# Optimization experiments

Measured on AMD Instinct MI355X. Metric: run time of the kernel, lower is better.

## Reference

```python
import jax, jax.numpy as jnp
import numpy as np

BASE_THETA = 0.5
K_DOP = 0.2
K_NOR = 0.15
K_SERO = 0.1
DIM = 1024


def setup_inputs() -> dict:
    key = jax.random.key(0)
    ks = jax.random.split(key, 9)
    scale = 1.0 / np.sqrt(DIM)
    x = jax.random.normal(ks[0], (2, 2048, DIM), dtype=jnp.float32)
    Wq = jax.random.normal(ks[1], (DIM, DIM), dtype=jnp.float32) * scale
    bq = jnp.zeros((DIM,), dtype=jnp.float32)
    Wk = jax.random.normal(ks[2], (DIM, DIM), dtype=jnp.float32) * scale
    bk = jnp.zeros((DIM,), dtype=jnp.float32)
    Wv = jax.random.normal(ks[3], (DIM, DIM), dtype=jnp.float32) * scale
    bv = jnp.zeros((DIM,), dtype=jnp.float32)
    Wo = jax.random.normal(ks[4], (DIM, DIM), dtype=jnp.float32) * scale
    bo = jnp.zeros((DIM,), dtype=jnp.float32)
    return {"x": x, "Wq": Wq, "bq": bq, "Wk": Wk, "bk": bk,
            "Wv": Wv, "bv": bv, "Wo": Wo, "bo": bo}


def reference(x, Wq, bq, Wk, bk, Wv, bv, Wo, bo):
    # Projections: torch nn.Linear computes x @ W.T + b
    q = jnp.einsum('bsd,ed->bse', x, Wq) + bq
    k = jnp.einsum('bsd,ed->bse', x, Wk) + bk
    v = jnp.einsum('bsd,ed->bse', x, Wv) + bv
    # Full [B, S, S] scores (no 1/sqrt(d) scaling in the original)
    qk = jnp.einsum('bsd,btd->bst', q, k)
    theta = (BASE_THETA
             + K_DOP * jax.nn.sigmoid(qk)
             + K_NOR * jnp.tanh(qk)
             + K_SERO * jax.nn.relu(qk))
    attn = jax.nn.softmax(theta, axis=-1)
    out = jnp.einsum('bst,btd->bsd', attn, v)
    return jnp.einsum('bsd,ed->bse', out, Wo) + bo
```

## Files before the change

kernel.cpp:

```cpp
#include <hip/hip_runtime.h>
#include <hip/hip_fp16.h>
#include <stdint.h>

typedef _Float16 f16;
typedef __attribute__((ext_vector_type(8))) _Float16 f16x8;
typedef __attribute__((ext_vector_type(4))) _Float16 f16x4;
typedef __attribute__((ext_vector_type(4))) float f32x4;

#define SEQ 2048
#define DIM 1024
#define NBATCH 2
#define MTOT 4096

__global__ void fill_kernel(float* p, float v, int n){
  int i = blockIdx.x * 256 + threadIdx.x;
  if (i < n) p[i] = v;
}

__global__ void cvt_all(const float* __restrict__ x, const float* __restrict__ Wq,
                        const float* __restrict__ Wk, const float* __restrict__ Wv,
                        const float* __restrict__ Wo, const float* __restrict__ bo,
                        f16* __restrict__ x16, f16* __restrict__ Wcat, f16* __restrict__ Wo16,
                        float* __restrict__ rowacc, float* __restrict__ out){
  int b = blockIdx.x;
  if (b >= 8193){
    const long i = (long)(b - 8193) * 256 + threadIdx.x;
    ((float4*)out)[i] = ((const float4*)bo)[i & 255];
    return;
  }
  if (b == 8192){
    float4 z = {0.f, 0.f, 0.f, 0.f};
#pragma unroll
    for (int i = 0; i < 4; i++) ((float4*)rowacc)[threadIdx.x + i * 256] = z;
    return;
  }
  const float* src; f16* dst; int i;
  if (b < 4096){
    src = x; dst = x16; i = b * 256 + threadIdx.x;
  } else {
    int t = (b - 4096) >> 10;
    i = ((b - 4096) & 1023) * 256 + threadIdx.x;
    src = t == 0 ? Wq : t == 1 ? Wk : t == 2 ? Wv : Wo;
    dst = (t == 3) ? Wo16 : Wcat + (size_t)t * DIM * DIM;
  }
  float4 v = ((const float4*)src)[i];
  ((f16x4*)dst)[i] = (f16x4){(f16)v.x, (f16)v.y, (f16)v.z, (f16)v.w};
}

#define GLOAD16(SRC, DST) __builtin_amdgcn_global_load_lds( \
    (__attribute__((address_space(1))) void*)(SRC), \
    (__attribute__((address_space(3))) void*)(DST), 16, 0, 0)

__device__ __forceinline__ float theta_exp(float v){
  const float e1 = __expf(-v);
  const float sg = 1.f / (1.f + e1);
  const float e2 = e1 * e1;
  const float th = 2.f / (1.f + e2) - 1.f;
  const float theta = 0.5f + 0.2f * sg + 0.15f * th + 0.1f * fmaxf(v, 0.f);
  return __expf(fminf(theta - 10.f, 11.f));
}

__global__ __launch_bounds__(256, 3)
void gemm_qkv(const f16* __restrict__ A0, const f16* __restrict__ B0,
              f16* __restrict__ O0, f16* __restrict__ O1,
              const float* __restrict__ c0, const float* __restrict__ c1,
              const float* __restrict__ c2)
{
  __shared__ __align__(16) f16 As[8192];
  __shared__ __align__(16) f16 Bs[8192];
  const int tid  = threadIdx.x;
  const int lane = tid & 63;
  const int wid  = tid >> 6;
  const int bm = blockIdx.x, bn = blockIdx.y;

  const int s_r  = tid >> 3;
  const int s_cb = (tid & 7) ^ (s_r & 7);
  const f16* Ab = A0 + (long)(bm * 128 + s_r) * DIM + s_cb * 8;
  const f16* Bb = B0 + (long)(bn * 128 + s_r) * DIM + s_cb * 8;

  const int l15 = lane & 15, l7 = lane & 7, lhi = lane >> 4;
  const int wrow = (wid >> 1) * 64;
  const int wcol = (wid & 1) * 64;
  const int ar = (wrow + l15) * 64;
  const int br = (wcol + l15) * 64;
  const int cb0 = ((0 + lhi) ^ l7) * 8;
  const int cb1 = ((4 + lhi) ^ l7) * 8;

  f32x4 acc[4][4] = {};

#pragma unroll
  for (int t = 0; t < 16; ++t){
    __syncthreads();
    GLOAD16(Ab + (long)t*64,                  &As[       tid*8]);
    GLOAD16(Ab + (long)t*64 + (long)32 * DIM, &As[2048 + tid*8]);
    GLOAD16(Ab + (long)t*64 + (long)64 * DIM, &As[4096 + tid*8]);
    GLOAD16(Ab + (long)t*64 + (long)96 * DIM, &As[6144 + tid*8]);
    GLOAD16(Bb + (long)t*64,                  &Bs[       tid*8]);
    GLOAD16(Bb + (long)t*64 + (long)32 * DIM, &Bs[2048 + tid*8]);
    GLOAD16(Bb + (long)t*64 + (long)64 * DIM, &Bs[4096 + tid*8]);
    GLOAD16(Bb + (long)t*64 + (long)96 * DIM, &Bs[6144 + tid*8]);
    __syncthreads();
    f16x8 af[4], bf[4];
#pragma unroll
    for (int i = 0; i < 4; i++) af[i] = *(const f16x8*)&As[ar + i * 1024 + cb0];
#pragma unroll
    for (int j = 0; j < 4; j++) bf[j] = *(const f16x8*)&Bs[br + j * 1024 + cb0];
#pragma unroll
    for (int i = 0; i < 4; i++)
#pragma unroll
      for (int j = 0; j < 4; j++)
        acc[i][j] = __builtin_amdgcn_mfma_f32_16x16x32_f16(af[i], bf[j], acc[i][j], 0, 0, 0);
#pragma unroll
    for (int i = 0; i < 4; i++) af[i] = *(const f16x8*)&As[ar + i * 1024 + cb1];
#pragma unroll
    for (int j = 0; j < 4; j++) bf[j] = *(const f16x8*)&Bs[br + j * 1024 + cb1];
#pragma unroll
    for (int i = 0; i < 4; i++)
#pragma unroll
      for (int j = 0; j < 4; j++)
        acc[i][j] = __builtin_amdgcn_mfma_f32_16x16x32_f16(af[i], bf[j], acc[i][j], 0, 0, 0);
  }

  const int cc = l15;
  const int rr = lhi * 4;
#pragma unroll
  for (int i = 0; i < 4; i++)
#pragma unroll
    for (int j = 0; j < 4; j++){
      const int col = bn * 128 + wcol + j * 16 + cc;
      if (col < 2048){
        const float badd = (col < 1024) ? c0[col] : c1[col - 1024];
#pragma unroll
        for (int r = 0; r < 4; r++){
          const int row = bm * 128 + wrow + i * 16 + rr + r;
          O0[(long)row * 2048 + col] = (f16)(acc[i][j][r] + badd);
        }
      } else {
        const int dcol = col - 2048;
        const float badd = c2[dcol];
#pragma unroll
        for (int r = 0; r < 4; r++){
          const int row = bm * 128 + wrow + i * 16 + rr + r;
          O1[(long)row * DIM + dcol] = (f16)(acc[i][j][r] + badd);
        }
      }
    }
}

__global__ __launch_bounds__(256, 3)
void gemm_merged(const f16* __restrict__ qkcat, const f16* __restrict__ vbuf,
                 const f16* __restrict__ Wo16,
                 f16* __restrict__ Pbuf, f16* __restrict__ vWoT,
                 float* __restrict__ rowacc)
{
  __shared__ __align__(16) f16 As[8192];
  __shared__ __align__(16) f16 Bs[8192];
  const int tid  = threadIdx.x;
  const int lane = tid & 63;
  const int wid  = tid >> 6;
  const int l15 = lane & 15, l7 = lane & 7, lhi = lane >> 4;
  const int s_r  = tid >> 3;
  const int s_cb = (tid & 7) ^ (s_r & 7);
  const int cb0 = ((0 + lhi) ^ l7) * 8;
  const int cb1 = ((4 + lhi) ^ l7) * 8;
  const int cc = l15, rr = lhi * 4;
  const int wrow = (wid >> 1) * 64;
  const int wcol = (wid & 1) * 64;
  const int ar = (wrow + l15) * 64;
  const int br = (wcol + l15) * 64;
  const int r = blockIdx.x;

  if (r < 512){
    const int x = r & 7, i5 = r >> 3;
    const int bz = x >> 2;
    const int bn = (x & 3) * 4 + (i5 & 3);
    const int bm = i5 >> 2;
    const f16* Ab = qkcat + (long)bz * SEQ * 2048 + (long)(bm * 128 + s_r) * 2048 + s_cb * 8;
    const f16* Bb = qkcat + DIM + (long)bz * SEQ * 2048 + (long)(bn * 128 + s_r) * 2048 + s_cb * 8;

    f32x4 acc[4][4] = {};

#pragma unroll
    for (int t = 0; t < 16; ++t){
      __syncthreads();
      GLOAD16(Ab + (long)t*64,                   &As[       tid*8]);
      GLOAD16(Ab + (long)t*64 + (long)32 * 2048, &As[2048 + tid*8]);
      GLOAD16(Ab + (long)t*64 + (long)64 * 2048, &As[4096 + tid*8]);
      GLOAD16(Ab + (long)t*64 + (long)96 * 2048, &As[6144 + tid*8]);
      GLOAD16(Bb + (long)t*64,                   &Bs[       tid*8]);
      GLOAD16(Bb + (long)t*64 + (long)32 * 2048, &Bs[2048 + tid*8]);
      GLOAD16(Bb + (long)t*64 + (long)64 * 2048, &Bs[4096 + tid*8]);
      GLOAD16(Bb + (long)t*64 + (long)96 * 2048, &Bs[6144 + tid*8]);
      __syncthreads();
      f16x8 af[4], bf[4];
#pragma unroll
      for (int i = 0; i < 4; i++) af[i] = *(const f16x8*)&As[ar + i * 1024 + cb0];
#pragma unroll
      for (int j = 0; j < 4; j++) bf[j] = *(const f16x8*)&Bs[br + j * 1024 + cb0];
#pragma unroll
      for (int i = 0; i < 4; i++)
#pragma unroll
        for (int j = 0; j < 4; j++)
          acc[i][j] = __builtin_amdgcn_mfma_f32_16x16x32_f16(af[i], bf[j], acc[i][j], 0, 0, 0);
#pragma unroll
      for (int i = 0; i < 4; i++) af[i] = *(const f16x8*)&As[ar + i * 1024 + cb1];
#pragma unroll
      for (int j = 0; j < 4; j++) bf[j] = *(const f16x8*)&Bs[br + j * 1024 + cb1];
#pragma unroll
      for (int i = 0; i < 4; i++)
#pragma unroll
        for (int j = 0; j < 4; j++)
          acc[i][j] = __builtin_amdgcn_mfma_f32_16x16x32_f16(af[i], bf[j], acc[i][j], 0, 0, 0);
    }

#pragma unroll
    for (int i = 0; i < 4; i++)
#pragma unroll
      for (int rq = 0; rq < 4; rq++){
        const int row = bm * 128 + wrow + i * 16 + rr + rq;
        float rs = 0.f;
#pragma unroll
        for (int j = 0; j < 4; j++){
          const int col = bn * 128 + wcol + j * 16 + cc;
          const float P = theta_exp(acc[i][j][rq]);
          Pbuf[(long)bz * SEQ * SEQ + (long)row * SEQ + col] = (f16)P;
          rs += P;
        }
        rs += __shfl_xor(rs, 1, 64);
        rs += __shfl_xor(rs, 2, 64);
        rs += __shfl_xor(rs, 4, 64);
        rs += __shfl_xor(rs, 8, 64);
        if (cc == 0) atomicAdd(&rowacc[bz * SEQ + row], rs);
      }
  } else {
    const int rr2 = r - 512;
    const int x = rr2 & 7, i5 = rr2 >> 3;
    const int bz = x >> 2;
    const int bn = (x & 3) * 2 + (i5 & 1);
    const int bm = i5 >> 1;
    const f16* Ab = vbuf + (long)bz * SEQ * DIM + (long)(bm * 128 + s_r) * DIM + s_cb * 8;
    const f16* Bb = Wo16 + (long)(bn * 128 + s_r) * DIM + s_cb * 8;

    f32x4 acc[4][4] = {};

#pragma unroll
    for (int t = 0; t < 16; ++t){
      __syncthreads();
      GLOAD16(Ab + (long)t*64,                  &As[       tid*8]);
      GLOAD16(Ab + (long)t*64 + (long)32 * DIM, &As[2048 + tid*8]);
      GLOAD16(Ab + (long)t*64 + (long)64 * DIM, &As[4096 + tid*8]);
      GLOAD16(Ab + (long)t*64 + (long)96 * DIM, &As[6144 + tid*8]);
      GLOAD16(Bb + (long)t*64,                  &Bs[       tid*8]);
      GLOAD16(Bb + (long)t*64 + (long)32 * DIM, &Bs[2048 + tid*8]);
      GLOAD16(Bb + (long)t*64 + (long)64 * DIM, &Bs[4096 + tid*8]);
      GLOAD16(Bb + (long)t*64 + (long)96 * DIM, &Bs[6144 + tid*8]);
      __syncthreads();
      f16x8 af[4], bf[4];
#pragma unroll
      for (int i = 0; i < 4; i++) af[i] = *(const f16x8*)&As[ar + i * 1024 + cb0];
#pragma unroll
      for (int j = 0; j < 4; j++) bf[j] = *(const f16x8*)&Bs[br + j * 1024 + cb0];
#pragma unroll
      for (int i = 0; i < 4; i++)
#pragma unroll
        for (int j = 0; j < 4; j++)
          acc[i][j] = __builtin_amdgcn_mfma_f32_16x16x32_f16(af[i], bf[j], acc[i][j], 0, 0, 0);
#pragma unroll
      for (int i = 0; i < 4; i++) af[i] = *(const f16x8*)&As[ar + i * 1024 + cb1];
#pragma unroll
      for (int j = 0; j < 4; j++) bf[j] = *(const f16x8*)&Bs[br + j * 1024 + cb1];
#pragma unroll
      for (int i = 0; i < 4; i++)
#pragma unroll
        for (int j = 0; j < 4; j++)
          acc[i][j] = __builtin_amdgcn_mfma_f32_16x16x32_f16(af[i], bf[j], acc[i][j], 0, 0, 0);
    }

#pragma unroll
    for (int i = 0; i < 4; i++)
#pragma unroll
      for (int j = 0; j < 4; j++){
        const int col = bn * 128 + wcol + j * 16 + cc;
        const int row0 = bm * 128 + wrow + i * 16 + rr;
        f16x4 pk = {(f16)acc[i][j][0], (f16)acc[i][j][1],
                    (f16)acc[i][j][2], (f16)acc[i][j][3]};
        *(f16x4*)&vWoT[(long)bz * DIM * SEQ + (long)col * SEQ + row0] = pk;
      }
  }
}

__global__ __launch_bounds__(256, 2)
void gemm_final(const f16* __restrict__ Pb, const f16* __restrict__ Vw,
                float* __restrict__ out, const float* __restrict__ rowacc)
{
  __shared__ __align__(16) f16 As[8192];
  __shared__ __align__(16) f16 Bs[8192];
  const int tid  = threadIdx.x;
  const int lane = tid & 63;
  const int wid  = tid >> 6;
  const int r = blockIdx.x;
  const int x = r & 7, i5 = r >> 3;
  const int z4 = x >> 1;
  const int bz = z4 >> 1, kh = z4 & 1;
  const int bn = (x & 1) * 4 + (i5 & 3);
  const int bm = i5 >> 2;

  const f16* Ag = Pb + (long)bz * SEQ * SEQ + (long)kh * 1024;
  const f16* Bg = Vw + (long)bz * DIM * SEQ + (long)kh * 1024;

  const int s_r  = tid >> 3;
  const int s_cb = (tid & 7) ^ (s_r & 7);
  const f16* Ab = Ag + (long)(bm * 128 + s_r) * 2048 + s_cb * 8;
  const f16* Bb = Bg + (long)(bn * 128 + s_r) * 2048 + s_cb * 8;

  const int l15 = lane & 15, l7 = lane & 7, lhi = lane >> 4;
  const int wrow = (wid >> 1) * 64;
  const int wcol = (wid & 1) * 64;
  const int ar = (wrow + l15) * 64;
  const int br = (wcol + l15) * 64;
  const int cb0 = ((0 + lhi) ^ l7) * 8;
  const int cb1 = ((4 + lhi) ^ l7) * 8;

  f32x4 acc[4][4] = {};

#pragma unroll
  for (int t = 0; t < 16; ++t){
    __syncthreads();
    GLOAD16(Ab + (long)t*64,                   &As[       tid*8]);
    GLOAD16(Ab + (long)t*64 + (long)32 * 2048, &As[2048 + tid*8]);
    GLOAD16(Ab + (long)t*64 + (long)64 * 2048, &As[4096 + tid*8]);
    GLOAD16(Ab + (long)t*64 + (long)96 * 2048, &As[6144 + tid*8]);
    GLOAD16(Bb + (long)t*64,                   &Bs[       tid*8]);
    GLOAD16(Bb + (long)t*64 + (long)32 * 2048, &Bs[2048 + tid*8]);
    GLOAD16(Bb + (long)t*64 + (long)64 * 2048, &Bs[4096 + tid*8]);
    GLOAD16(Bb + (long)t*64 + (long)96 * 2048, &Bs[6144 + tid*8]);
    __syncthreads();
    f16x8 af[4], bf[4];
#pragma unroll
    for (int i = 0; i < 4; i++) af[i] = *(const f16x8*)&As[ar + i * 1024 + cb0];
#pragma unroll
    for (int j = 0; j < 4; j++) bf[j] = *(const f16x8*)&Bs[br + j * 1024 + cb0];
#pragma unroll
    for (int i = 0; i < 4; i++)
#pragma unroll
      for (int j = 0; j < 4; j++)
        acc[i][j] = __builtin_amdgcn_mfma_f32_16x16x32_f16(af[i], bf[j], acc[i][j], 0, 0, 0);
#pragma unroll
    for (int i = 0; i < 4; i++) af[i] = *(const f16x8*)&As[ar + i * 1024 + cb1];
#pragma unroll
    for (int j = 0; j < 4; j++) bf[j] = *(const f16x8*)&Bs[br + j * 1024 + cb1];
#pragma unroll
    for (int i = 0; i < 4; i++)
#pragma unroll
      for (int j = 0; j < 4; j++)
        acc[i][j] = __builtin_amdgcn_mfma_f32_16x16x32_f16(af[i], bf[j], acc[i][j], 0, 0, 0);
  }

  const int cc = l15;
  const int rr = lhi * 4;
  float* Ob = out + (long)bz * SEQ * DIM;
#pragma unroll
  for (int i = 0; i < 4; i++)
#pragma unroll
    for (int r4 = 0; r4 < 4; r4++){
      const int row = bm * 128 + wrow + i * 16 + rr + r4;
      const float inv = 1.f / rowacc[bz * SEQ + row];
#pragma unroll
      for (int j = 0; j < 4; j++){
        const int col = bn * 128 + wcol + j * 16 + cc;
        atomicAdd(&Ob[(long)row * DIM + col], acc[i][j][r4] * inv);
      }
    }
}

extern "C" void kernel_launch(void* const* d_in, const int* in_sizes, int n_in,
                              void* d_out, int out_size, void* d_ws, size_t ws_size,
                              hipStream_t stream){
  const float* x  = (const float*)d_in[0];
  const float* Wq = (const float*)d_in[1];
  const float* bq = (const float*)d_in[2];
  const float* Wk = (const float*)d_in[3];
  const float* bk = (const float*)d_in[4];
  const float* Wv = (const float*)d_in[5];
  const float* bv = (const float*)d_in[6];
  const float* Wo = (const float*)d_in[7];
  const float* bo = (const float*)d_in[8];
  float* out = (float*)d_out;

  char* ws = (char*)d_ws;
  size_t off = 0;
  auto alloc = [&](size_t bytes) -> char* {
    char* p = ws + off; off += (bytes + 255) & ~(size_t)255; return p;
  };

  f16* x16     = (f16*)alloc(2ull * MTOT * DIM);
  f16* Wcat    = (f16*)alloc(2ull * 3 * DIM * DIM);
  f16* Wo16    = (f16*)alloc(2ull * DIM * DIM);
  f16* qkcat   = (f16*)alloc(2ull * MTOT * 2 * DIM);
  f16* vbuf    = (f16*)alloc(2ull * MTOT * DIM);
  f16* Pbuf    = (f16*)alloc(2ull * NBATCH * SEQ * SEQ);
  f16* vWoT    = (f16*)alloc(2ull * NBATCH * DIM * SEQ);
  float* rowac = (float*)alloc(4ull * MTOT);

  if (off > ws_size){
    fill_kernel<<<(out_size + 255) / 256, 256, 0, stream>>>(out, 12345.0f, out_size);
    return;
  }

  cvt_all<<<12289, 256, 0, stream>>>(x, Wq, Wk, Wv, Wo, bo,
                                     x16, Wcat, Wo16, rowac, out);

  gemm_qkv<<<dim3(MTOT / 128, 3 * DIM / 128, 1), 256, 0, stream>>>(
      x16, Wcat, qkcat, vbuf, bq, bk, bv);

  gemm_merged<<<768, 256, 0, stream>>>(qkcat, vbuf, Wo16, Pbuf, vWoT, rowac);

  gemm_final<<<512, 256, 0, stream>>>(Pbuf, vWoT, out, rowac);
}
```

Baseline: 127.7 us.

## Replace atomic accumulation with split-K partial buffers and a combine kernel

Stops computing softmax row sums with atomics in the score GEMM and instead sums the f16 P values inside the final GEMM (only bn==0 tiles write them). The final GEMM now writes plain float partials per K-half rather than atomically adding normalized values into the output. A new combine kernel adds the two halves, normalizes by the row sums and adds the bias. This removes float atomics and the output and rowacc pre-fill, at the cost of an extra 32 MB partial buffer round trip, an extra launch, and some extra adds in the GEMM loop. The grid ordering in gemm_final changes and the occupancy hint rises to 4.

```diff
diff --git a/kernel.cpp b/kernel.cpp
--- a/kernel.cpp
+++ b/kernel.cpp
@@ -19,21 +19,9 @@
 
 __global__ void cvt_all(const float* __restrict__ x, const float* __restrict__ Wq,
                         const float* __restrict__ Wk, const float* __restrict__ Wv,
-                        const float* __restrict__ Wo, const float* __restrict__ bo,
-                        f16* __restrict__ x16, f16* __restrict__ Wcat, f16* __restrict__ Wo16,
-                        float* __restrict__ rowacc, float* __restrict__ out){
+                        const float* __restrict__ Wo,
+                        f16* __restrict__ x16, f16* __restrict__ Wcat, f16* __restrict__ Wo16){
   int b = blockIdx.x;
-  if (b >= 8193){
-    const long i = (long)(b - 8193) * 256 + threadIdx.x;
-    ((float4*)out)[i] = ((const float4*)bo)[i & 255];
-    return;
-  }
-  if (b == 8192){
-    float4 z = {0.f, 0.f, 0.f, 0.f};
-#pragma unroll
-    for (int i = 0; i < 4; i++) ((float4*)rowacc)[threadIdx.x + i * 256] = z;
-    return;
-  }
   const float* src; f16* dst; int i;
   if (b < 4096){
     src = x; dst = x16; i = b * 256 + threadIdx.x;
@@ -150,8 +138,7 @@
 __global__ __launch_bounds__(256, 3)
 void gemm_merged(const f16* __restrict__ qkcat, const f16* __restrict__ vbuf,
                  const f16* __restrict__ Wo16,
-                 f16* __restrict__ Pbuf, f16* __restrict__ vWoT,
-                 float* __restrict__ rowacc)
+                 f16* __restrict__ Pbuf, f16* __restrict__ vWoT)
 {
   __shared__ __align__(16) f16 As[8192];
   __shared__ __align__(16) f16 Bs[8192];
@@ -218,19 +205,11 @@
 #pragma unroll
       for (int rq = 0; rq < 4; rq++){
         const int row = bm * 128 + wrow + i * 16 + rr + rq;
-        float rs = 0.f;
 #pragma unroll
         for (int j = 0; j < 4; j++){
           const int col = bn * 128 + wcol + j * 16 + cc;
-          const float P = theta_exp(acc[i][j][rq]);
-          Pbuf[(long)bz * SEQ * SEQ + (long)row * SEQ + col] = (f16)P;
-          rs += P;
+          Pbuf[(long)bz * SEQ * SEQ + (long)row * SEQ + col] = (f16)theta_exp(acc[i][j][rq]);
         }
-        rs += __shfl_xor(rs, 1, 64);
-        rs += __shfl_xor(rs, 2, 64);
-        rs += __shfl_xor(rs, 4, 64);
-        rs += __shfl_xor(rs, 8, 64);
-        if (cc == 0) atomicAdd(&rowacc[bz * SEQ + row], rs);
       }
   } else {
     const int rr2 = r - 512;
@@ -289,21 +268,17 @@
   }
 }
 
-__global__ __launch_bounds__(256, 2)
+__global__ __launch_bounds__(256, 4)
 void gemm_final(const f16* __restrict__ Pb, const f16* __restrict__ Vw,
-                float* __restrict__ out, const float* __restrict__ rowacc)
+                float* __restrict__ psum, float* __restrict__ rowsum)
 {
   __shared__ __align__(16) f16 As[8192];
   __shared__ __align__(16) f16 Bs[8192];
   const int tid  = threadIdx.x;
   const int lane = tid & 63;
   const int wid  = tid >> 6;
-  const int r = blockIdx.x;
-  const int x = r & 7, i5 = r >> 3;
-  const int z4 = x >> 1;
-  const int bz = z4 >> 1, kh = z4 & 1;
-  const int bn = (x & 1) * 4 + (i5 & 3);
-  const int bm = i5 >> 2;
+  const int bm = blockIdx.x, bn = blockIdx.y;
+  const int bz = blockIdx.z >> 1, kh = blockIdx.z & 1;
 
   const f16* Ag = Pb + (long)bz * SEQ * SEQ + (long)kh * 1024;
   const f16* Bg = Vw + (long)bz * DIM * SEQ + (long)kh * 1024;
@@ -320,8 +295,10 @@
   const int br = (wcol + l15) * 64;
   const int cb0 = ((0 + lhi) ^ l7) * 8;
   const int cb1 = ((4 + lhi) ^ l7) * 8;
+  const bool do_rs = ((wid & 1) == 0);
 
   f32x4 acc[4][4] = {};
+  float rsum[4] = {0.f, 0.f, 0.f, 0.f};
 
 #pragma unroll
   for (int t = 0; t < 16; ++t){
@@ -345,6 +322,12 @@
 #pragma unroll
       for (int j = 0; j < 4; j++)
         acc[i][j] = __builtin_amdgcn_mfma_f32_16x16x32_f16(af[i], bf[j], acc[i][j], 0, 0, 0);
+    if (do_rs){
+#pragma unroll
+      for (int i = 0; i < 4; i++)
+#pragma unroll
+        for (int e = 0; e < 8; e++) rsum[i] += (float)af[i][e];
+    }
 #pragma unroll
     for (int i = 0; i < 4; i++) af[i] = *(const f16x8*)&As[ar + i * 1024 + cb1];
 #pragma unroll
@@ -354,23 +337,60 @@
 #pragma unroll
       for (int j = 0; j < 4; j++)
         acc[i][j] = __builtin_amdgcn_mfma_f32_16x16x32_f16(af[i], bf[j], acc[i][j], 0, 0, 0);
+    if (do_rs){
+#pragma unroll
+      for (int i = 0; i < 4; i++)
+#pragma unroll
+        for (int e = 0; e < 8; e++) rsum[i] += (float)af[i][e];
+    }
+  }
+
+  if (do_rs){
+#pragma unroll
+    for (int i = 0; i < 4; i++){
+      rsum[i] += __shfl_xor(rsum[i], 16, 64);
+      rsum[i] += __shfl_xor(rsum[i], 32, 64);
+    }
+    if (bn == 0 && lane < 16){
+#pragma unroll
+      for (int i = 0; i < 4; i++)
+        rowsum[(long)kh * MTOT + bz * SEQ + bm * 128 + wrow + i * 16 + lane] = rsum[i];
+    }
   }
 
   const int cc = l15;
   const int rr = lhi * 4;
-  float* Ob = out + (long)bz * SEQ * DIM;
+  float* Po = psum + (long)kh * MTOT * DIM + (long)bz * SEQ * DIM;
 #pragma unroll
   for (int i = 0; i < 4; i++)
 #pragma unroll
-    for (int r4 = 0; r4 < 4; r4++){
-      const int row = bm * 128 + wrow + i * 16 + rr + r4;
-      const float inv = 1.f / rowacc[bz * SEQ + row];
-#pragma unroll
-      for (int j = 0; j < 4; j++){
-        const int col = bn * 128 + wcol + j * 16 + cc;
-        atomicAdd(&Ob[(long)row * DIM + col], acc[i][j][r4] * inv);
+    for (int j = 0; j < 4; j++){
+      const int col = bn * 128 + wcol + j * 16 + cc;
+#pragma unroll
+      for (int r = 0; r < 4; r++){
+        const int row = bm * 128 + wrow + i * 16 + rr + r;
+        Po[(long)row * DIM + col] = acc[i][j][r];
       }
     }
+}
+
+__global__ __launch_bounds__(256)
+void combine_kernel(const float* __restrict__ psum, const float* __restrict__ rowsum,
+                    const float* __restrict__ bo, float* __restrict__ out)
+{
+  const long i = (long)blockIdx.x * 256 + threadIdx.x;
+  const int row = (int)(i >> 8);
+  const int c4  = (int)(i & 255);
+  float4 a = ((const float4*)psum)[i];
+  float4 b = ((const float4*)psum)[i + (long)MTOT * DIM / 4];
+  float4 bb = ((const float4*)bo)[c4];
+  const float inv = 1.f / (rowsum[row] + rowsum[MTOT + row]);
+  float4 o;
+  o.x = (a.x + b.x) * inv + bb.x;
+  o.y = (a.y + b.y) * inv + bb.y;
+  o.z = (a.z + b.z) * inv + bb.z;
+  o.w = (a.w + b.w) * inv + bb.w;
+  ((float4*)out)[i] = o;
 }
 
 extern "C" void kernel_launch(void* const* d_in, const int* in_sizes, int n_in,
@@ -400,20 +420,23 @@
   f16* vbuf    = (f16*)alloc(2ull * MTOT * DIM);
   f16* Pbuf    = (f16*)alloc(2ull * NBATCH * SEQ * SEQ);
   f16* vWoT    = (f16*)alloc(2ull * NBATCH * DIM * SEQ);
-  float* rowac = (float*)alloc(4ull * MTOT);
+  float* psum  = (float*)alloc(4ull * 2 * MTOT * DIM);
+  float* rowsm = (float*)alloc(4ull * 2 * MTOT);
 
   if (off > ws_size){
     fill_kernel<<<(out_size + 255) / 256, 256, 0, stream>>>(out, 12345.0f, out_size);
     return;
   }
 
-  cvt_all<<<12289, 256, 0, stream>>>(x, Wq, Wk, Wv, Wo, bo,
-                                     x16, Wcat, Wo16, rowac, out);
+  cvt_all<<<8192, 256, 0, stream>>>(x, Wq, Wk, Wv, Wo, x16, Wcat, Wo16);
 
   gemm_qkv<<<dim3(MTOT / 128, 3 * DIM / 128, 1), 256, 0, stream>>>(
       x16, Wcat, qkcat, vbuf, bq, bk, bv);
 
-  gemm_merged<<<768, 256, 0, stream>>>(qkcat, vbuf, Wo16, Pbuf, vWoT, rowac);
-
-  gemm_final<<<512, 256, 0, stream>>>(Pbuf, vWoT, out, rowac);
-}
+  gemm_merged<<<768, 256, 0, stream>>>(qkcat, vbuf, Wo16, Pbuf, vWoT);
+
+  gemm_final<<<dim3(SEQ / 128, DIM / 128, 2 * NBATCH), 256, 0, stream>>>(
+      Pbuf, vWoT, psum, rowsm);
+
+  combine_kernel<<<MTOT * DIM / 4 / 256, 256, 0, stream>>>(psum, rowsm, bo, out);
+}
```

Measured after the change: 120.9 us. -5.4%, faster.
